# Kernel tuning notes

Measured on AMD Instinct MI355X. Metric: run time of the kernel, lower is better.

## Reference

```python
import jax, jax.numpy as jnp
import numpy as np

NUM_HEAD = 2
KR = 3          # kernel_range = [3, 3]
SHIFT = 1
N_P = KR * KR   # 9 taps
PAD = (KR // 2) * SHIFT  # 1
OFFSETS = [(i, j) for i in (-(KR // 2), 0, KR // 2) if True for j in ()]  # placeholder, real list below
OFFSETS = [(i, j) for i in range(-(KR // 2), KR // 2 + 1) for j in range(-(KR // 2), KR // 2 + 1)]


def _conv3x3(x, w, b):
    # x: [B,H,W,Cin], w: [3,3,Cin,Cout] -> SAME conv + bias
    y = jax.lax.conv_general_dilated(
        x, w, window_strides=(1, 1), padding='SAME',
        dimension_numbers=('NHWC', 'HWIO', 'NHWC'))
    return y + b


def setup_inputs() -> dict:
    key = jax.random.key(0)
    B, H, W, D = 4, 128, 128, 64
    ks = jax.random.split(key, 10)
    sc = 0.05  # small init like glorot
    return {
        'x': jax.random.normal(ks[0], (B, H, W, D), jnp.float32),
        # 1x1 conv kernels stored as matrices (equiv. to (1,1,Cin,Cout))
        'K_P': jax.random.normal(ks[1], (D, D * N_P), jnp.float32) * sc,
        'V_P': jax.random.normal(ks[2], (D, D * N_P), jnp.float32) * sc,
        'Q_P': jax.random.normal(ks[3], (D, D), jnp.float32) * sc,
        'ff1_kernel': jax.random.normal(ks[4], (D, D), jnp.float32) * sc,
        'ff1_bias': jax.random.normal(ks[5], (D,), jnp.float32) * sc,
        'ff2_kernel': jax.random.normal(ks[6], (3, 3, D, 2 * D), jnp.float32) * sc,
        'ff2_bias': jax.random.normal(ks[7], (2 * D,), jnp.float32) * sc,
        'ff3_kernel': jax.random.normal(ks[8], (3, 3, 2 * D, D), jnp.float32) * sc,
        'ff3_bias': jax.random.normal(ks[9], (D,), jnp.float32) * sc,
    }


def reference(x, K_P, V_P, Q_P, ff1_kernel, ff1_bias, ff2_kernel, ff2_bias,
              ff3_kernel, ff3_bias):
    B, H, W, D = x.shape
    hd = D // NUM_HEAD

    # 1x1 projections; K/V produce N_P channel chunks, one per tap
    x_k = jnp.einsum('bhwd,de->bhwe', x, K_P).reshape(B, H, W, N_P, D)
    x_v = jnp.einsum('bhwd,de->bhwe', x, V_P).reshape(B, H, W, N_P, D)
    x_q = jnp.einsum('bhwd,de->bhwe', x, Q_P)

    pad5 = ((0, 0), (PAD, PAD), (PAD, PAD), (0, 0), (0, 0))
    k_pad = jnp.pad(x_k, pad5)
    v_pad = jnp.pad(x_v, pad5)

    # tap t uses channel chunk t at spatial offset OFFSETS[t]*SHIFT
    def taps(padded):
        return jnp.stack(
            [padded[:, PAD + i * SHIFT:PAD + i * SHIFT + H,
                    PAD + j * SHIFT:PAD + j * SHIFT + W, t, :]
             for t, (i, j) in enumerate(OFFSETS)], axis=3)  # [B,H,W,N_P,D]

    k_taps = taps(k_pad)
    v_taps = taps(v_pad)

    # validity mask (padded taps get score 0 before softmax, as in original)
    m_pad = jnp.pad(jnp.ones((B, H, W), x.dtype), ((0, 0), (PAD, PAD), (PAD, PAD)))
    mask = jnp.stack(
        [m_pad[:, PAD + i * SHIFT:PAD + i * SHIFT + H,
               PAD + j * SHIFT:PAD + j * SHIFT + W]
         for (i, j) in OFFSETS], axis=3)  # [B,H,W,N_P]

    kh = k_taps.reshape(B, H, W, N_P, NUM_HEAD, hd)
    vh = v_taps.reshape(B, H, W, N_P, NUM_HEAD, hd)
    qh = x_q.reshape(B, H, W, NUM_HEAD, hd)

    # scores per head over taps; masked-multiply then /3, as in original
    scores = jnp.einsum('bhwtnc,bhwnc->bhwnt', kh, qh)
    scores = scores * mask[:, :, :, None, :] / 3.0
    alpha = jax.nn.softmax(scores, axis=-1)  # over taps
    attn = jnp.einsum('bhwnt,bhwtnc->bhwnc', alpha, vh).reshape(B, H, W, D)

    # FFN: 1x1 conv -> relu -> 3x3 conv -> relu -> 3x3 conv -> relu
    t = jax.nn.relu(jnp.einsum('bhwd,de->bhwe', attn, ff1_kernel) + ff1_bias)
    t = jax.nn.relu(_conv3x3(t, ff2_kernel, ff2_bias))
    t = jax.nn.relu(_conv3x3(t, ff3_kernel, ff3_bias))
    return t
```

## Files before the change

kernel.cpp:

```cpp
#include <hip/hip_runtime.h>


typedef _Float16 half8 __attribute__((ext_vector_type(8)));
typedef _Float16 half4v __attribute__((ext_vector_type(4)));
typedef float f32x4 __attribute__((ext_vector_type(4)));

__device__ __forceinline__ f32x4 mfma16(half8 a, half8 b, f32x4 c) {
  return __builtin_amdgcn_mfma_f32_16x16x32_f16(a, b, c, 0, 0, 0);
}
__device__ __forceinline__ half8 ldfrag(const _Float16* p) { return *(const half8*)p; }
__device__ __forceinline__ half8 zfrag() { half8 z = {}; return z; }

__device__ __forceinline__ void gload_lds16(const _Float16* g, _Float16* l) {
  __builtin_amdgcn_global_load_lds(
      (const __attribute__((address_space(1))) void*)g,
      (__attribute__((address_space(3))) void*)l, 16, 0, 0);
}

__global__ __launch_bounds__(256) void prep(
    const float* __restrict__ x, const float* __restrict__ Kp,
    const float* __restrict__ Vp, const float* __restrict__ Qp,
    const float* __restrict__ W1, const float* __restrict__ F2,
    const float* __restrict__ F3, _Float16* __restrict__ xh,
    _Float16* __restrict__ out) {
  if (blockIdx.x < 4096) {
    int i = blockIdx.x * 256 + threadIdx.x;
    float4 v = ((const float4*)x)[i];
    half4v h = { (_Float16)v.x, (_Float16)v.y, (_Float16)v.z, (_Float16)v.w };
    *(half4v*)(xh + i * 4) = h;
    return;
  }
  int e = (blockIdx.x - 4096) * 256 + threadIdx.x;
  int j = e & 7, l = (e >> 3) & 63, f = e >> 9;
  int l15 = l & 15, q8 = (l >> 4) * 8;
  float v;
  if (f < 8)        { int mb = f >> 1, kb = f & 1;
                      v = Qp[(kb*32 + q8 + j) * 64 + mb*16 + l15]; }
  else if (f < 80)  { int g = f - 8, t = g >> 3, mb = (g >> 1) & 3, kb = g & 1;
                      v = Kp[(kb*32 + q8 + j) * 576 + t*64 + mb*16 + l15]; }
  else if (f < 152) { int g = f - 80, t = g >> 3, kb = (g >> 2) & 1, nb = g & 3;
                      v = Vp[(kb*32 + q8 + j) * 576 + t*64 + nb*16 + l15]; }
  else if (f < 160) { int g = f - 152, kb = g >> 2, nb = g & 3;
                      v = W1[(kb*32 + q8 + j) * 64 + nb*16 + l15]; }
  else if (f < 304) { int g = f - 160, t = g >> 4, kb = (g >> 3) & 1, nb = g & 7;
                      v = F2[(t*64 + kb*32 + q8 + j) * 128 + nb*16 + l15]; }
  else              { int g = f - 304, t = g >> 4, kb = (g >> 2) & 3, nb = g & 3;
                      v = F3[(t*128 + kb*32 + q8 + j) * 64 + nb*16 + l15]; }
  out[e] = (_Float16)v;
}

__global__ __launch_bounds__(512) void attn_ff1(
    const _Float16* __restrict__ xh, const _Float16* __restrict__ wf,
    const float* __restrict__ f1b, _Float16* __restrict__ t1g) {
  extern __shared__ _Float16 smem[];
  const int lane = threadIdx.x & 63, wid = threadIdx.x >> 6;
  const int l15 = lane & 15, q8 = (lane >> 4) * 8;
  const int row = blockIdx.x * 2 + (wid >> 2);
  const int rw = wid & 3;
  const int p0 = row * 128 + rw * 32;
  const int h = row & 127;
  const int w0 = rw * 32;
  float* dent = (float*)(smem + 77824) + wid * 64;

  {
    const _Float16* gw = wf + 4096 + (size_t)(wid * 19) * 512;
    _Float16* lw = smem + wid * 19 * 512;
    for (int i = 0; i < 19; ++i)
      gload_lds16(gw + i * 512 + lane * 8, lw + i * 512);
  }

  half8 ax0[2], ax1[2];
#pragma unroll
  for (int m = 0; m < 2; ++m) {
    const _Float16* xp = xh + (size_t)(p0 + m * 16 + l15) * 64 + q8;
    ax0[m] = ldfrag(xp); ax1[m] = ldfrag(xp + 32);
  }
  f32x4 qT[2][4];
#pragma unroll
  for (int cb = 0; cb < 4; ++cb) {
    half8 aq0 = ldfrag(wf + (cb * 2 + 0) * 512 + lane * 8);
    half8 aq1 = ldfrag(wf + (cb * 2 + 1) * 512 + lane * 8);
#pragma unroll
    for (int m = 0; m < 2; ++m) {
      f32x4 c = {};
      c = mfma16(aq0, ax0[m], c);
      c = mfma16(aq1, ax1[m], c);
      qT[m][cb] = c;
    }
  }

  auto load_tap = [&](int t, half8 (&x0)[2], half8 (&x1)[2]) {
    const int dh = t / 3 - 1, dw = t % 3 - 1;
    const bool rk = (unsigned)(h + dh) < 128u;
#pragma unroll
    for (int m = 0; m < 2; ++m) {
      const bool cv = rk && ((unsigned)(w0 + m * 16 + l15 + dw) < 128u);
      const _Float16* sp = xh + (size_t)(p0 + m * 16 + l15 + dh * 128 + dw) * 64 + q8;
      x0[m] = cv ? ldfrag(sp) : zfrag();
      x1[m] = cv ? ldfrag(sp + 32) : zfrag();
    }
  };

  float den0[2] = {0.f, 0.f}, den1[2] = {0.f, 0.f};
  auto score_tap = [&](int t, half8 (&x0)[2], half8 (&x1)[2],
                       float (&e0)[2], float (&e1)[2]) {
    const int dh = t / 3 - 1;
    const bool rowok = (unsigned)(h + dh) < 128u;
#pragma unroll
    for (int m = 0; m < 2; ++m) {
      float pa = 0.f, pb = 0.f;
      if (rowok) {
#pragma unroll
        for (int cb = 0; cb < 4; ++cb) {
          f32x4 c = {};
          c = mfma16(ldfrag(smem + (t * 8 + cb * 2 + 0) * 512 + lane * 8), x0[m], c);
          c = mfma16(ldfrag(smem + (t * 8 + cb * 2 + 1) * 512 + lane * 8), x1[m], c);
          float d = qT[m][cb].x * c.x + qT[m][cb].y * c.y
                  + qT[m][cb].z * c.z + qT[m][cb].w * c.w;
          if (cb < 2) pa += d; else pb += d;
        }
        pa += __shfl_xor(pa, 16, 64); pa += __shfl_xor(pa, 32, 64);
        pb += __shfl_xor(pb, 16, 64); pb += __shfl_xor(pb, 32, 64);
      }
      e0[m] = __expf(pa * (1.f / 3.f));
      e1[m] = __expf(pb * (1.f / 3.f));
      den0[m] += e0[m]; den1[m] += e1[m];
    }
  };

  half8 sx0[2], sx1[2];
  load_tap(0, sx0, sx1);

  __syncthreads();

  float e0c[2], e1c[2];
  score_tap(0, sx0, sx1, e0c, e1c);

  const _Float16* BVl = smem + 36864;
  f32x4 at[2][4];
#pragma unroll
  for (int m = 0; m < 2; ++m)
#pragma unroll
    for (int nb = 0; nb < 4; ++nb) at[m][nb] = f32x4{};

#pragma unroll
  for (int t = 0; t < 9; ++t) {
    const bool rowok = (unsigned)(h + (t / 3 - 1)) < 128u;
    half8 nx0[2], nx1[2];
    if (t < 8) load_tap(t + 1, nx0, nx1);
    if (rowok) {
      half8 vf[8];
#pragma unroll
      for (int f = 0; f < 8; ++f) vf[f] = ldfrag(BVl + (t * 8 + f) * 512 + lane * 8);
#pragma unroll
      for (int m = 0; m < 2; ++m) {
        _Float16 h0 = (_Float16)e0c[m], h1 = (_Float16)e1c[m];
        half8 b0 = {h0, h0, h0, h0, h0, h0, h0, h0};
        half8 b1 = {h1, h1, h1, h1, h1, h1, h1, h1};
        half8 s00 = sx0[m] * b0, s01 = sx1[m] * b0;
        half8 s10 = sx0[m] * b1, s11 = sx1[m] * b1;
#pragma unroll
        for (int nb = 0; nb < 2; ++nb) {
          at[m][nb]     = mfma16(s00, vf[0 * 4 + nb],     at[m][nb]);
          at[m][nb]     = mfma16(s01, vf[1 * 4 + nb],     at[m][nb]);
          at[m][nb + 2] = mfma16(s10, vf[0 * 4 + nb + 2], at[m][nb + 2]);
          at[m][nb + 2] = mfma16(s11, vf[1 * 4 + nb + 2], at[m][nb + 2]);
        }
      }
    }
    if (t < 8) {
      float e0n[2], e1n[2];
      score_tap(t + 1, nx0, nx1, e0n, e1n);
#pragma unroll
      for (int m = 0; m < 2; ++m) {
        sx0[m] = nx0[m]; sx1[m] = nx1[m];
        e0c[m] = e0n[m]; e1c[m] = e1n[m];
      }
    }
  }

#pragma unroll
  for (int m = 0; m < 2; ++m) {
    dent[(m * 2 + 0) * 16 + l15] = den0[m];
    dent[(m * 2 + 1) * 16 + l15] = den1[m];
  }
  f32x4 iv[2][2];
#pragma unroll
  for (int m = 0; m < 2; ++m)
#pragma unroll
    for (int hd = 0; hd < 2; ++hd) {
      f32x4 dv = *(const f32x4*)(dent + (m * 2 + hd) * 16 + (lane >> 4) * 4);
      iv[m][hd] = f32x4{1.f / dv.x, 1.f / dv.y, 1.f / dv.z, 1.f / dv.w};
    }

  __syncthreads();
  _Float16* myt = smem + wid * 2304;
#pragma unroll
  for (int m = 0; m < 2; ++m)
#pragma unroll
    for (int nb = 0; nb < 4; ++nb) {
      const int hd = nb >> 1;
#pragma unroll
      for (int r = 0; r < 4; ++r)
        myt[m * 1152 + ((lane >> 4) * 4 + r) * 72 + nb * 16 + l15] =
            (_Float16)(at[m][nb][r] * iv[m][hd][r]);
    }
  const _Float16* B1l = smem + 73728;
#pragma unroll
  for (int m = 0; m < 2; ++m) {
    half8 aa0 = ldfrag(myt + m * 1152 + l15 * 72 + q8);
    half8 aa1 = ldfrag(myt + m * 1152 + l15 * 72 + 32 + q8);
#pragma unroll
    for (int nb = 0; nb < 4; ++nb) {
      f32x4 c = {};
      c = mfma16(aa0, ldfrag(B1l + (0 * 4 + nb) * 512 + lane * 8), c);
      c = mfma16(aa1, ldfrag(B1l + (1 * 4 + nb) * 512 + lane * 8), c);
      float bv = f1b[nb * 16 + l15];
#pragma unroll
      for (int r = 0; r < 4; ++r) {
        float v = fmaxf(c[r] + bv, 0.f);
        t1g[(size_t)(p0 + m * 16 + (lane >> 4) * 4 + r) * 64 + nb * 16 + l15] = (_Float16)v;
      }
    }
  }
}

template <int KB, int NBL, int COUT>
__global__ __launch_bounds__(512, 2) void conv3x3(
    const _Float16* __restrict__ in, const _Float16* __restrict__ wfrag,
    const float* __restrict__ bias, void* __restrict__ outp, int out_fp32) {
  extern __shared__ _Float16 smem[];
  const int lane = threadIdx.x & 63, wid = threadIdx.x >> 6;
  const int l15 = lane & 15, q8 = (lane >> 4) * 8;
  const int nh = blockIdx.x & 1;
  const int pairIdx = blockIdx.x >> 1;
  const int row = pairIdx * 2 + (wid >> 2);
  const int rw = wid & 3;
  const int p0 = row * 128 + rw * 32;
  const int h = row & 127;
  const int w0 = rw * 32;
  const int CIN = KB * 32;
  const int NBF = COUT / 16;

  {
    for (int s = 0; s < 9; ++s) {
      int f = wid * 9 + s;
      int t = f >> 3, r = f & 7, kb = r / NBL, i = r % NBL;
      const _Float16* g = wfrag + (size_t)((t * KB + kb) * NBF + nh * NBL + i) * 512;
      gload_lds16(g + lane * 8, smem + f * 512);
    }
  }

  f32x4 acc[2][NBL];
#pragma unroll
  for (int m = 0; m < 2; ++m)
#pragma unroll
    for (int nb = 0; nb < NBL; ++nb) acc[m][nb] = f32x4{};

  half8 a[2][KB];
  {
    const bool rk = (unsigned)(h - 1) < 128u;
#pragma unroll
    for (int m = 0; m < 2; ++m) {
      const bool cv = rk && ((unsigned)(w0 + m * 16 + l15 - 1) < 128u);
      const _Float16* sp = in + (size_t)(p0 + m * 16 + l15 - 129) * CIN + q8;
#pragma unroll
      for (int kb = 0; kb < KB; ++kb) a[m][kb] = cv ? ldfrag(sp + kb * 32) : zfrag();
    }
  }

  __syncthreads();

#pragma unroll
  for (int t = 0; t < 9; ++t) {
    const int dh = t / 3 - 1;
    const bool rowok = (unsigned)(h + dh) < 128u;
    half8 an[2][KB];
    if (t < 8) {
      const int dh2 = (t + 1) / 3 - 1, dw2 = (t + 1) % 3 - 1;
      const bool rk2 = (unsigned)(h + dh2) < 128u;
#pragma unroll
      for (int m = 0; m < 2; ++m) {
        const bool cv = rk2 && ((unsigned)(w0 + m * 16 + l15 + dw2) < 128u);
        const _Float16* sp = in + (size_t)(p0 + m * 16 + l15 + dh2 * 128 + dw2) * CIN + q8;
#pragma unroll
        for (int kb = 0; kb < KB; ++kb) an[m][kb] = cv ? ldfrag(sp + kb * 32) : zfrag();
      }
    }
    if (rowok) {
#pragma unroll
      for (int nb = 0; nb < NBL; ++nb) {
#pragma unroll
        for (int kb = 0; kb < KB; ++kb) {
          half8 b = ldfrag(smem + (size_t)((t * KB + kb) * NBL + nb) * 512 + lane * 8);
          acc[0][nb] = mfma16(a[0][kb], b, acc[0][nb]);
          acc[1][nb] = mfma16(a[1][kb], b, acc[1][nb]);
        }
      }
    }
    if (t < 8) {
#pragma unroll
      for (int m = 0; m < 2; ++m)
#pragma unroll
        for (int kb = 0; kb < KB; ++kb) a[m][kb] = an[m][kb];
    }
  }

#pragma unroll
  for (int m = 0; m < 2; ++m)
#pragma unroll
    for (int nb = 0; nb < NBL; ++nb) {
      float bv = bias[nh * NBL * 16 + nb * 16 + l15];
#pragma unroll
      for (int r = 0; r < 4; ++r) {
        float v = fmaxf(acc[m][nb][r] + bv, 0.f);
        size_t idx = (size_t)(p0 + m * 16 + (lane >> 4) * 4 + r) * COUT
                   + nh * NBL * 16 + nb * 16 + l15;
        if (out_fp32) ((float*)outp)[idx] = v;
        else          ((_Float16*)outp)[idx] = (_Float16)v;
      }
    }
}

extern "C" void kernel_launch(void* const* d_in, const int* in_sizes, int n_in,
                              void* d_out, int out_size, void* d_ws, size_t ws_size,
                              hipStream_t stream) {
  (void)in_sizes; (void)n_in; (void)out_size; (void)ws_size;
  const float* x   = (const float*)d_in[0];
  const float* Kp  = (const float*)d_in[1];
  const float* Vp  = (const float*)d_in[2];
  const float* Qp  = (const float*)d_in[3];
  const float* f1w = (const float*)d_in[4];
  const float* f1b = (const float*)d_in[5];
  const float* f2w = (const float*)d_in[6];
  const float* f2b = (const float*)d_in[7];
  const float* f3w = (const float*)d_in[8];
  const float* f3b = (const float*)d_in[9];

  _Float16* xh  = (_Float16*)d_ws;
  _Float16* wf  = xh + 4194304;
  _Float16* t2g = wf + 229376;
  _Float16* t1g = (_Float16*)d_out;

  (void)hipFuncSetAttribute((const void*)attn_ff1,
      hipFuncAttributeMaxDynamicSharedMemorySize, 157696);
  (void)hipFuncSetAttribute((const void*)conv3x3<2, 4, 128>,
      hipFuncAttributeMaxDynamicSharedMemorySize, 73728);
  (void)hipFuncSetAttribute((const void*)conv3x3<4, 2, 64>,
      hipFuncAttributeMaxDynamicSharedMemorySize, 73728);

  prep<<<4992, 256, 0, stream>>>(x, Kp, Vp, Qp, f1w, f2w, f3w, xh, wf);
  attn_ff1<<<256, 512, 157696, stream>>>(xh, wf, f1b, t1g);
  conv3x3<2, 4, 128><<<512, 512, 73728, stream>>>(t1g, wf + 81920, f2b, t2g, 0);
  conv3x3<4, 2, 64><<<512, 512, 73728, stream>>>(t2g, wf + 155648, f3b, d_out, 1);
}
```

Measured before the change: 166.0 us.

## Fuse all four stages into one cooperative persistent kernel with grid syncs

Replaces the four separate launches (prep, attention+ff1, two 3x3 convs) with one cooperative kernel of 256 blocks that runs each stage in turn, separated by grid-wide syncs. This removes launch gaps and inter-kernel drain. Each conv stage now has one block compute all output channels for two rows, where before two blocks split the channels, which halves parallelism in the conv stages. With 157KB of LDS per block the grid runs at one block per CU, so occupancy drops and the grid syncs add their own overhead.

Result: slower. 255.6 us (+53.9%).

```diff
diff --git a/kernel.cpp b/kernel.cpp
--- a/kernel.cpp
+++ b/kernel.cpp
@@ -1,4 +1,6 @@
 #include <hip/hip_runtime.h>
+#include <hip/hip_cooperative_groups.h>
+namespace cg = cooperative_groups;
 
 
 typedef _Float16 half8 __attribute__((ext_vector_type(8)));
@@ -17,41 +19,102 @@
       (__attribute__((address_space(3))) void*)l, 16, 0, 0);
 }
 
-__global__ __launch_bounds__(256) void prep(
+template <int KB, int NB, bool OUT_FP32>
+__device__ __forceinline__ void conv_stage(
+    _Float16* smem, const _Float16* __restrict__ in,
+    const _Float16* __restrict__ wfrag, const float* __restrict__ bias,
+    void* __restrict__ outp, int lane, int wid, int row, int rw) {
+  const int l15 = lane & 15, q8 = (lane >> 4) * 8;
+  const int p0 = row * 128 + rw * 32;
+  const int h = row & 127;
+  const int w0 = rw * 32;
+  const int CIN = KB * 32, COUT = NB * 16;
+
+#pragma unroll
+  for (int i = 0; i < 18; ++i) {
+    int f = wid * 18 + i;
+    gload_lds16(wfrag + (size_t)f * 512 + lane * 8, smem + f * 512);
+  }
+
+  f32x4 acc[2][NB];
+#pragma unroll
+  for (int m = 0; m < 2; ++m)
+#pragma unroll
+    for (int nb = 0; nb < NB; ++nb) acc[m][nb] = f32x4{};
+
+  half8 a[2][KB];
+  {
+    const bool rk = (unsigned)(h - 1) < 128u;
+#pragma unroll
+    for (int m = 0; m < 2; ++m) {
+      const bool cv = rk && ((unsigned)(w0 + m * 16 + l15 - 1) < 128u);
+      const _Float16* sp = in + (size_t)(p0 + m * 16 + l15 - 129) * CIN + q8;
+#pragma unroll
+      for (int kb = 0; kb < KB; ++kb) a[m][kb] = cv ? ldfrag(sp + kb * 32) : zfrag();
+    }
+  }
+
+  __syncthreads();
+
+#pragma unroll
+  for (int t = 0; t < 9; ++t) {
+    const int dh = t / 3 - 1;
+    const bool rowok = (unsigned)(h + dh) < 128u;
+    half8 an[2][KB];
+    if (t < 8) {
+      const int dh2 = (t + 1) / 3 - 1, dw2 = (t + 1) % 3 - 1;
+      const bool rk2 = (unsigned)(h + dh2) < 128u;
+#pragma unroll
+      for (int m = 0; m < 2; ++m) {
+        const bool cv = rk2 && ((unsigned)(w0 + m * 16 + l15 + dw2) < 128u);
+        const _Float16* sp = in + (size_t)(p0 + m * 16 + l15 + dh2 * 128 + dw2) * CIN + q8;
+#pragma unroll
+        for (int kb = 0; kb < KB; ++kb) an[m][kb] = cv ? ldfrag(sp + kb * 32) : zfrag();
+      }
+    }
+    if (rowok) {
+#pragma unroll
+      for (int nb = 0; nb < NB; ++nb) {
+#pragma unroll
+        for (int kb = 0; kb < KB; ++kb) {
+          half8 b = ldfrag(smem + (size_t)((t * KB + kb) * NB + nb) * 512 + lane * 8);
+          acc[0][nb] = mfma16(a[0][kb], b, acc[0][nb]);
+          acc[1][nb] = mfma16(a[1][kb], b, acc[1][nb]);
+        }
+      }
+    }
+    if (t < 8) {
+#pragma unroll
+      for (int m = 0; m < 2; ++m)
+#pragma unroll
+        for (int kb = 0; kb < KB; ++kb) a[m][kb] = an[m][kb];
+    }
+  }
+
+#pragma unroll
+  for (int m = 0; m < 2; ++m)
+#pragma unroll
+    for (int nb = 0; nb < NB; ++nb) {
+      float bv = bias[nb * 16 + l15];
+#pragma unroll
+      for (int r = 0; r < 4; ++r) {
+        float v = fmaxf(acc[m][nb][r] + bv, 0.f);
+        size_t idx = (size_t)(p0 + m * 16 + (lane >> 4) * 4 + r) * COUT + nb * 16 + l15;
+        if (OUT_FP32) ((float*)outp)[idx] = v;
+        else          ((_Float16*)outp)[idx] = (_Float16)v;
+      }
+    }
+}
+
+__global__ __launch_bounds__(512) void fused(
     const float* __restrict__ x, const float* __restrict__ Kp,
     const float* __restrict__ Vp, const float* __restrict__ Qp,
-    const float* __restrict__ W1, const float* __restrict__ F2,
-    const float* __restrict__ F3, _Float16* __restrict__ xh,
-    _Float16* __restrict__ out) {
-  if (blockIdx.x < 4096) {
-    int i = blockIdx.x * 256 + threadIdx.x;
-    float4 v = ((const float4*)x)[i];
-    half4v h = { (_Float16)v.x, (_Float16)v.y, (_Float16)v.z, (_Float16)v.w };
-    *(half4v*)(xh + i * 4) = h;
-    return;
-  }
-  int e = (blockIdx.x - 4096) * 256 + threadIdx.x;
-  int j = e & 7, l = (e >> 3) & 63, f = e >> 9;
-  int l15 = l & 15, q8 = (l >> 4) * 8;
-  float v;
-  if (f < 8)        { int mb = f >> 1, kb = f & 1;
-                      v = Qp[(kb*32 + q8 + j) * 64 + mb*16 + l15]; }
-  else if (f < 80)  { int g = f - 8, t = g >> 3, mb = (g >> 1) & 3, kb = g & 1;
-                      v = Kp[(kb*32 + q8 + j) * 576 + t*64 + mb*16 + l15]; }
-  else if (f < 152) { int g = f - 80, t = g >> 3, kb = (g >> 2) & 1, nb = g & 3;
-                      v = Vp[(kb*32 + q8 + j) * 576 + t*64 + nb*16 + l15]; }
-  else if (f < 160) { int g = f - 152, kb = g >> 2, nb = g & 3;
-                      v = W1[(kb*32 + q8 + j) * 64 + nb*16 + l15]; }
-  else if (f < 304) { int g = f - 160, t = g >> 4, kb = (g >> 3) & 1, nb = g & 7;
-                      v = F2[(t*64 + kb*32 + q8 + j) * 128 + nb*16 + l15]; }
-  else              { int g = f - 304, t = g >> 4, kb = (g >> 2) & 3, nb = g & 3;
-                      v = F3[(t*128 + kb*32 + q8 + j) * 64 + nb*16 + l15]; }
-  out[e] = (_Float16)v;
-}
-
-__global__ __launch_bounds__(512) void attn_ff1(
-    const _Float16* __restrict__ xh, const _Float16* __restrict__ wf,
-    const float* __restrict__ f1b, _Float16* __restrict__ t1g) {
+    const float* __restrict__ W1, const float* __restrict__ f1b,
+    const float* __restrict__ F2, const float* __restrict__ f2b,
+    const float* __restrict__ F3, const float* __restrict__ f3b,
+    _Float16* __restrict__ xh, _Float16* __restrict__ wf,
+    _Float16* __restrict__ t1g, _Float16* __restrict__ t2g,
+    float* __restrict__ outp) {
   extern __shared__ _Float16 smem[];
   const int lane = threadIdx.x & 63, wid = threadIdx.x >> 6;
   const int l15 = lane & 15, q8 = (lane >> 4) * 8;
@@ -60,266 +123,213 @@
   const int p0 = row * 128 + rw * 32;
   const int h = row & 127;
   const int w0 = rw * 32;
-  float* dent = (float*)(smem + 77824) + wid * 64;
+  const int gtid = blockIdx.x * 512 + threadIdx.x;
 
   {
-    const _Float16* gw = wf + 4096 + (size_t)(wid * 19) * 512;
-    _Float16* lw = smem + wid * 19 * 512;
-    for (int i = 0; i < 19; ++i)
-      gload_lds16(gw + i * 512 + lane * 8, lw + i * 512);
-  }
-
-  half8 ax0[2], ax1[2];
-#pragma unroll
-  for (int m = 0; m < 2; ++m) {
-    const _Float16* xp = xh + (size_t)(p0 + m * 16 + l15) * 64 + q8;
-    ax0[m] = ldfrag(xp); ax1[m] = ldfrag(xp + 32);
-  }
-  f32x4 qT[2][4];
-#pragma unroll
-  for (int cb = 0; cb < 4; ++cb) {
-    half8 aq0 = ldfrag(wf + (cb * 2 + 0) * 512 + lane * 8);
-    half8 aq1 = ldfrag(wf + (cb * 2 + 1) * 512 + lane * 8);
+    const float4* x4 = (const float4*)x;
+#pragma unroll
+    for (int k = 0; k < 8; ++k) {
+      int i = gtid + k * 131072;
+      float4 v = x4[i];
+      half4v hv = { (_Float16)v.x, (_Float16)v.y, (_Float16)v.z, (_Float16)v.w };
+      *(half4v*)(xh + (size_t)i * 4) = hv;
+    }
+#pragma unroll
+    for (int k = 0; k < 2; ++k) {
+      int e = gtid + k * 131072;
+      if (e < 229376) {
+        int j = e & 7, l = (e >> 3) & 63, f = e >> 9;
+        int ll = l & 15, qq = (l >> 4) * 8;
+        float v;
+        if (f < 8)        { int mb = f >> 1, kb = f & 1;
+                            v = Qp[(kb*32 + qq + j) * 64 + mb*16 + ll]; }
+        else if (f < 80)  { int g = f - 8, t = g >> 3, mb = (g >> 1) & 3, kb = g & 1;
+                            v = Kp[(kb*32 + qq + j) * 576 + t*64 + mb*16 + ll]; }
+        else if (f < 152) { int g = f - 80, t = g >> 3, kb = (g >> 2) & 1, nb = g & 3;
+                            v = Vp[(kb*32 + qq + j) * 576 + t*64 + nb*16 + ll]; }
+        else if (f < 160) { int g = f - 152, kb = g >> 2, nb = g & 3;
+                            v = W1[(kb*32 + qq + j) * 64 + nb*16 + ll]; }
+        else if (f < 304) { int g = f - 160, t = g >> 4, kb = (g >> 3) & 1, nb = g & 7;
+                            v = F2[(t*64 + kb*32 + qq + j) * 128 + nb*16 + ll]; }
+        else              { int g = f - 304, t = g >> 4, kb = (g >> 2) & 3, nb = g & 3;
+                            v = F3[(t*128 + kb*32 + qq + j) * 64 + nb*16 + ll]; }
+        wf[e] = (_Float16)v;
+      }
+    }
+  }
+  cg::this_grid().sync();
+
+  {
+    float* dent = (float*)(smem + 77824) + wid * 64;
+
+    {
+      const _Float16* gw = wf + 4096 + (size_t)(wid * 19) * 512;
+      _Float16* lw = smem + wid * 19 * 512;
+      for (int i = 0; i < 19; ++i)
+        gload_lds16(gw + i * 512 + lane * 8, lw + i * 512);
+    }
+
+    half8 ax0[2], ax1[2];
 #pragma unroll
     for (int m = 0; m < 2; ++m) {
-      f32x4 c = {};
-      c = mfma16(aq0, ax0[m], c);
-      c = mfma16(aq1, ax1[m], c);
-      qT[m][cb] = c;
-    }
-  }
-
-  auto load_tap = [&](int t, half8 (&x0)[2], half8 (&x1)[2]) {
-    const int dh = t / 3 - 1, dw = t % 3 - 1;
-    const bool rk = (unsigned)(h + dh) < 128u;
+      const _Float16* xp = xh + (size_t)(p0 + m * 16 + l15) * 64 + q8;
+      ax0[m] = ldfrag(xp); ax1[m] = ldfrag(xp + 32);
+    }
+    f32x4 qT[2][4];
+#pragma unroll
+    for (int cb = 0; cb < 4; ++cb) {
+      half8 aq0 = ldfrag(wf + (cb * 2 + 0) * 512 + lane * 8);
+      half8 aq1 = ldfrag(wf + (cb * 2 + 1) * 512 + lane * 8);
+#pragma unroll
+      for (int m = 0; m < 2; ++m) {
+        f32x4 c = {};
+        c = mfma16(aq0, ax0[m], c);
+        c = mfma16(aq1, ax1[m], c);
+        qT[m][cb] = c;
+      }
+    }
+
+    auto load_tap = [&](int t, half8 (&x0)[2], half8 (&x1)[2]) {
+      const int dh = t / 3 - 1, dw = t % 3 - 1;
+      const bool rk = (unsigned)(h + dh) < 128u;
+#pragma unroll
+      for (int m = 0; m < 2; ++m) {
+        const bool cv = rk && ((unsigned)(w0 + m * 16 + l15 + dw) < 128u);
+        const _Float16* sp = xh + (size_t)(p0 + m * 16 + l15 + dh * 128 + dw) * 64 + q8;
+        x0[m] = cv ? ldfrag(sp) : zfrag();
+        x1[m] = cv ? ldfrag(sp + 32) : zfrag();
+      }
+    };
+
+    float den0[2] = {0.f, 0.f}, den1[2] = {0.f, 0.f};
+    auto score_tap = [&](int t, half8 (&x0)[2], half8 (&x1)[2],
+                         float (&e0)[2], float (&e1)[2]) {
+      const int dh = t / 3 - 1;
+      const bool rowok = (unsigned)(h + dh) < 128u;
+#pragma unroll
+      for (int m = 0; m < 2; ++m) {
+        float pa = 0.f, pb = 0.f;
+        if (rowok) {
+#pragma unroll
+          for (int cb = 0; cb < 4; ++cb) {
+            f32x4 c = {};
+            c = mfma16(ldfrag(smem + (t * 8 + cb * 2 + 0) * 512 + lane * 8), x0[m], c);
+            c = mfma16(ldfrag(smem + (t * 8 + cb * 2 + 1) * 512 + lane * 8), x1[m], c);
+            float d = qT[m][cb].x * c.x + qT[m][cb].y * c.y
+                    + qT[m][cb].z * c.z + qT[m][cb].w * c.w;
+            if (cb < 2) pa += d; else pb += d;
+          }
+          pa += __shfl_xor(pa, 16, 64); pa += __shfl_xor(pa, 32, 64);
+          pb += __shfl_xor(pb, 16, 64); pb += __shfl_xor(pb, 32, 64);
+        }
+        e0[m] = __expf(pa * (1.f / 3.f));
+        e1[m] = __expf(pb * (1.f / 3.f));
+        den0[m] += e0[m]; den1[m] += e1[m];
+      }
+    };
+
+    half8 sx0[2], sx1[2];
+    load_tap(0, sx0, sx1);
+
+    __syncthreads();
+
+    float e0c[2], e1c[2];
+    score_tap(0, sx0, sx1, e0c, e1c);
+
+    const _Float16* BVl = smem + 36864;
+    f32x4 at[2][4];
+#pragma unroll
+    for (int m = 0; m < 2; ++m)
+#pragma unroll
+      for (int nb = 0; nb < 4; ++nb) at[m][nb] = f32x4{};
+
+#pragma unroll
+    for (int t = 0; t < 9; ++t) {
+      const bool rowok = (unsigned)(h + (t / 3 - 1)) < 128u;
+      half8 nx0[2], nx1[2];
+      if (t < 8) load_tap(t + 1, nx0, nx1);
+      if (rowok) {
+        half8 vf[8];
+#pragma unroll
+        for (int f = 0; f < 8; ++f) vf[f] = ldfrag(BVl + (t * 8 + f) * 512 + lane * 8);
+#pragma unroll
+        for (int m = 0; m < 2; ++m) {
+          _Float16 h0 = (_Float16)e0c[m], h1 = (_Float16)e1c[m];
+          half8 b0 = {h0, h0, h0, h0, h0, h0, h0, h0};
+          half8 b1 = {h1, h1, h1, h1, h1, h1, h1, h1};
+          half8 s00 = sx0[m] * b0, s01 = sx1[m] * b0;
+          half8 s10 = sx0[m] * b1, s11 = sx1[m] * b1;
+#pragma unroll
+          for (int nb = 0; nb < 2; ++nb) {
+            at[m][nb]     = mfma16(s00, vf[0 * 4 + nb],     at[m][nb]);
+            at[m][nb]     = mfma16(s01, vf[1 * 4 + nb],     at[m][nb]);
+            at[m][nb + 2] = mfma16(s10, vf[0 * 4 + nb + 2], at[m][nb + 2]);
+            at[m][nb + 2] = mfma16(s11, vf[1 * 4 + nb + 2], at[m][nb + 2]);
+          }
+        }
+      }
+      if (t < 8) {
+        float e0n[2], e1n[2];
+        score_tap(t + 1, nx0, nx1, e0n, e1n);
+#pragma unroll
+        for (int m = 0; m < 2; ++m) {
+          sx0[m] = nx0[m]; sx1[m] = nx1[m];
+          e0c[m] = e0n[m]; e1c[m] = e1n[m];
+        }
+      }
+    }
+
 #pragma unroll
     for (int m = 0; m < 2; ++m) {
-      const bool cv = rk && ((unsigned)(w0 + m * 16 + l15 + dw) < 128u);
-      const _Float16* sp = xh + (size_t)(p0 + m * 16 + l15 + dh * 128 + dw) * 64 + q8;
-      x0[m] = cv ? ldfrag(sp) : zfrag();
-      x1[m] = cv ? ldfrag(sp + 32) : zfrag();
-    }
-  };
-
-  float den0[2] = {0.f, 0.f}, den1[2] = {0.f, 0.f};
-  auto score_tap = [&](int t, half8 (&x0)[2], half8 (&x1)[2],
-                       float (&e0)[2], float (&e1)[2]) {
-    const int dh = t / 3 - 1;
-    const bool rowok = (unsigned)(h + dh) < 128u;
+      dent[(m * 2 + 0) * 16 + l15] = den0[m];
+      dent[(m * 2 + 1) * 16 + l15] = den1[m];
+    }
+    f32x4 iv[2][2];
+#pragma unroll
+    for (int m = 0; m < 2; ++m)
+#pragma unroll
+      for (int hd = 0; hd < 2; ++hd) {
+        f32x4 dv = *(const f32x4*)(dent + (m * 2 + hd) * 16 + (lane >> 4) * 4);
+        iv[m][hd] = f32x4{1.f / dv.x, 1.f / dv.y, 1.f / dv.z, 1.f / dv.w};
+      }
+
+    __syncthreads();
+    _Float16* myt = smem + wid * 2304;
+#pragma unroll
+    for (int m = 0; m < 2; ++m)
+#pragma unroll
+      for (int nb = 0; nb < 4; ++nb) {
+        const int hd = nb >> 1;
+#pragma unroll
+        for (int r = 0; r < 4; ++r)
+          myt[m * 1152 + ((lane >> 4) * 4 + r) * 72 + nb * 16 + l15] =
+              (_Float16)(at[m][nb][r] * iv[m][hd][r]);
+      }
+    const _Float16* B1l = smem + 73728;
 #pragma unroll
     for (int m = 0; m < 2; ++m) {
-      float pa = 0.f, pb = 0.f;
-      if (rowok) {
-#pragma unroll
-        for (int cb = 0; cb < 4; ++cb) {
-          f32x4 c = {};
-          c = mfma16(ldfrag(smem + (t * 8 + cb * 2 + 0) * 512 + lane * 8), x0[m], c);
-          c = mfma16(ldfrag(smem + (t * 8 + cb * 2 + 1) * 512 + lane * 8), x1[m], c);
-          float d = qT[m][cb].x * c.x + qT[m][cb].y * c.y
-                  + qT[m][cb].z * c.z + qT[m][cb].w * c.w;
-          if (cb < 2) pa += d; else pb += d;
-        }
-        pa += __shfl_xor(pa, 16, 64); pa += __shfl_xor(pa, 32, 64);
-        pb += __shfl_xor(pb, 16, 64); pb += __shfl_xor(pb, 32, 64);
-      }
-      e0[m] = __expf(pa * (1.f / 3.f));
-      e1[m] = __expf(pb * (1.f / 3.f));
-      den0[m] += e0[m]; den1[m] += e1[m];
-    }
-  };
-
-  half8 sx0[2], sx1[2];
-  load_tap(0, sx0, sx1);
-
-  __syncthreads();
-
-  float e0c[2], e1c[2];
-  score_tap(0, sx0, sx1, e0c, e1c);
-
-  const _Float16* BVl = smem + 36864;
-  f32x4 at[2][4];
-#pragma unroll
-  for (int m = 0; m < 2; ++m)
-#pragma unroll
-    for (int nb = 0; nb < 4; ++nb) at[m][nb] = f32x4{};
-
-#pragma unroll
-  for (int t = 0; t < 9; ++t) {
-    const bool rowok = (unsigned)(h + (t / 3 - 1)) < 128u;
-    half8 nx0[2], nx1[2];
-    if (t < 8) load_tap(t + 1, nx0, nx1);
-    if (rowok) {
-      half8 vf[8];
-#pragma unroll
-      for (int f = 0; f < 8; ++f) vf[f] = ldfrag(BVl + (t * 8 + f) * 512 + lane * 8);
-#pragma unroll
-      for (int m = 0; m < 2; ++m) {
-        _Float16 h0 = (_Float16)e0c[m], h1 = (_Float16)e1c[m];
-        half8 b0 = {h0, h0, h0, h0, h0, h0, h0, h0};
-        half8 b1 = {h1, h1, h1, h1, h1, h1, h1, h1};
-        half8 s00 = sx0[m] * b0, s01 = sx1[m] * b0;
-        half8 s10 = sx0[m] * b1, s11 = sx1[m] * b1;
-#pragma unroll
-        for (int nb = 0; nb < 2; ++nb) {
-          at[m][nb]     = mfma16(s00, vf[0 * 4 + nb],     at[m][nb]);
-          at[m][nb]     = mfma16(s01, vf[1 * 4 + nb],     at[m][nb]);
-          at[m][nb + 2] = mfma16(s10, vf[0 * 4 + nb + 2], at[m][nb + 2]);
-          at[m][nb + 2] = mfma16(s11, vf[1 * 4 + nb + 2], at[m][nb + 2]);
-        }
-      }
-    }
-    if (t < 8) {
-      float e0n[2], e1n[2];
-      score_tap(t + 1, nx0, nx1, e0n, e1n);
-#pragma unroll
-      for (int m = 0; m < 2; ++m) {
-        sx0[m] = nx0[m]; sx1[m] = nx1[m];
-        e0c[m] = e0n[m]; e1c[m] = e1n[m];
-      }
-    }
-  }
-
-#pragma unroll
-  for (int m = 0; m < 2; ++m) {
-    dent[(m * 2 + 0) * 16 + l15] = den0[m];
-    dent[(m * 2 + 1) * 16 + l15] = den1[m];
-  }
-  f32x4 iv[2][2];
-#pragma unroll
-  for (int m = 0; m < 2; ++m)
-#pragma unroll
-    for (int hd = 0; hd < 2; ++hd) {
-      f32x4 dv = *(const f32x4*)(dent + (m * 2 + hd) * 16 + (lane >> 4) * 4);
-      iv[m][hd] = f32x4{1.f / dv.x, 1.f / dv.y, 1.f / dv.z, 1.f / dv.w};
-    }
-
-  __syncthreads();
-  _Float16* myt = smem + wid * 2304;
-#pragma unroll
-  for (int m = 0; m < 2; ++m)
-#pragma unroll
-    for (int nb = 0; nb < 4; ++nb) {
-      const int hd = nb >> 1;
-#pragma unroll
-      for (int r = 0; r < 4; ++r)
-        myt[m * 1152 + ((lane >> 4) * 4 + r) * 72 + nb * 16 + l15] =
-            (_Float16)(at[m][nb][r] * iv[m][hd][r]);
-    }
-  const _Float16* B1l = smem + 73728;
-#pragma unroll
-  for (int m = 0; m < 2; ++m) {
-    half8 aa0 = ldfrag(myt + m * 1152 + l15 * 72 + q8);
-    half8 aa1 = ldfrag(myt + m * 1152 + l15 * 72 + 32 + q8);
-#pragma unroll
-    for (int nb = 0; nb < 4; ++nb) {
-      f32x4 c = {};
-      c = mfma16(aa0, ldfrag(B1l + (0 * 4 + nb) * 512 + lane * 8), c);
-      c = mfma16(aa1, ldfrag(B1l + (1 * 4 + nb) * 512 + lane * 8), c);
-      float bv = f1b[nb * 16 + l15];
-#pragma unroll
-      for (int r = 0; r < 4; ++r) {
-        float v = fmaxf(c[r] + bv, 0.f);
-        t1g[(size_t)(p0 + m * 16 + (lane >> 4) * 4 + r) * 64 + nb * 16 + l15] = (_Float16)v;
-      }
-    }
-  }
-}
-
-template <int KB, int NBL, int COUT>
-__global__ __launch_bounds__(512, 2) void conv3x3(
-    const _Float16* __restrict__ in, const _Float16* __restrict__ wfrag,
-    const float* __restrict__ bias, void* __restrict__ outp, int out_fp32) {
-  extern __shared__ _Float16 smem[];
-  const int lane = threadIdx.x & 63, wid = threadIdx.x >> 6;
-  const int l15 = lane & 15, q8 = (lane >> 4) * 8;
-  const int nh = blockIdx.x & 1;
-  const int pairIdx = blockIdx.x >> 1;
-  const int row = pairIdx * 2 + (wid >> 2);
-  const int rw = wid & 3;
-  const int p0 = row * 128 + rw * 32;
-  const int h = row & 127;
-  const int w0 = rw * 32;
-  const int CIN = KB * 32;
-  const int NBF = COUT / 16;
-
-  {
-    for (int s = 0; s < 9; ++s) {
-      int f = wid * 9 + s;
-      int t = f >> 3, r = f & 7, kb = r / NBL, i = r % NBL;
-      const _Float16* g = wfrag + (size_t)((t * KB + kb) * NBF + nh * NBL + i) * 512;
-      gload_lds16(g + lane * 8, smem + f * 512);
-    }
-  }
-
-  f32x4 acc[2][NBL];
-#pragma unroll
-  for (int m = 0; m < 2; ++m)
-#pragma unroll
-    for (int nb = 0; nb < NBL; ++nb) acc[m][nb] = f32x4{};
-
-  half8 a[2][KB];
-  {
-    const bool rk = (unsigned)(h - 1) < 128u;
-#pragma unroll
-    for (int m = 0; m < 2; ++m) {
-      const bool cv = rk && ((unsigned)(w0 + m * 16 + l15 - 1) < 128u);
-      const _Float16* sp = in + (size_t)(p0 + m * 16 + l15 - 129) * CIN + q8;
-#pragma unroll
-      for (int kb = 0; kb < KB; ++kb) a[m][kb] = cv ? ldfrag(sp + kb * 32) : zfrag();
-    }
-  }
-
-  __syncthreads();
-
-#pragma unroll
-  for (int t = 0; t < 9; ++t) {
-    const int dh = t / 3 - 1;
-    const bool rowok = (unsigned)(h + dh) < 128u;
-    half8 an[2][KB];
-    if (t < 8) {
-      const int dh2 = (t + 1) / 3 - 1, dw2 = (t + 1) % 3 - 1;
-      const bool rk2 = (unsigned)(h + dh2) < 128u;
-#pragma unroll
-      for (int m = 0; m < 2; ++m) {
-        const bool cv = rk2 && ((unsigned)(w0 + m * 16 + l15 + dw2) < 128u);
-        const _Float16* sp = in + (size_t)(p0 + m * 16 + l15 + dh2 * 128 + dw2) * CIN + q8;
-#pragma unroll
-        for (int kb = 0; kb < KB; ++kb) an[m][kb] = cv ? ldfrag(sp + kb * 32) : zfrag();
-      }
-    }
-    if (rowok) {
-#pragma unroll
-      for (int nb = 0; nb < NBL; ++nb) {
-#pragma unroll
-        for (int kb = 0; kb < KB; ++kb) {
-          half8 b = ldfrag(smem + (size_t)((t * KB + kb) * NBL + nb) * 512 + lane * 8);
-          acc[0][nb] = mfma16(a[0][kb], b, acc[0][nb]);
-          acc[1][nb] = mfma16(a[1][kb], b, acc[1][nb]);
-        }
-      }
-    }
-    if (t < 8) {
-#pragma unroll
-      for (int m = 0; m < 2; ++m)
-#pragma unroll
-        for (int kb = 0; kb < KB; ++kb) a[m][kb] = an[m][kb];
-    }
-  }
-
-#pragma unroll
-  for (int m = 0; m < 2; ++m)
-#pragma unroll
-    for (int nb = 0; nb < NBL; ++nb) {
-      float bv = bias[nh * NBL * 16 + nb * 16 + l15];
-#pragma unroll
-      for (int r = 0; r < 4; ++r) {
-        float v = fmaxf(acc[m][nb][r] + bv, 0.f);
-        size_t idx = (size_t)(p0 + m * 16 + (lane >> 4) * 4 + r) * COUT
-                   + nh * NBL * 16 + nb * 16 + l15;
-        if (out_fp32) ((float*)outp)[idx] = v;
-        else          ((_Float16*)outp)[idx] = (_Float16)v;
-      }
-    }
+      half8 aa0 = ldfrag(myt + m * 1152 + l15 * 72 + q8);
+      half8 aa1 = ldfrag(myt + m * 1152 + l15 * 72 + 32 + q8);
+#pragma unroll
+      for (int nb = 0; nb < 4; ++nb) {
+        f32x4 c = {};
+        c = mfma16(aa0, ldfrag(B1l + (0 * 4 + nb) * 512 + lane * 8), c);
+        c = mfma16(aa1, ldfrag(B1l + (1 * 4 + nb) * 512 + lane * 8), c);
+        float bv = f1b[nb * 16 + l15];
+#pragma unroll
+        for (int r = 0; r < 4; ++r) {
+          float v = fmaxf(c[r] + bv, 0.f);
+          t1g[(size_t)(p0 + m * 16 + (lane >> 4) * 4 + r) * 64 + nb * 16 + l15] = (_Float16)v;
+        }
+      }
+    }
+  }
+  cg::this_grid().sync();
+
+  conv_stage<2, 8, false>(smem, t1g, wf + 81920, f2b, t2g, lane, wid, row, rw);
+  cg::this_grid().sync();
+
+  conv_stage<4, 4, true>(smem, t2g, wf + 155648, f3b, outp, lane, wid, row, rw);
 }
 
 extern "C" void kernel_launch(void* const* d_in, const int* in_sizes, int n_in,
@@ -340,17 +350,16 @@
   _Float16* xh  = (_Float16*)d_ws;
   _Float16* wf  = xh + 4194304;
   _Float16* t2g = wf + 229376;
-  _Float16* t1g = (_Float16*)d_out;
-
-  (void)hipFuncSetAttribute((const void*)attn_ff1,
+  _Float16* t1g = t2g + 8388608;
+  float* outp = (float*)d_out;
+
+  (void)hipFuncSetAttribute((const void*)fused,
       hipFuncAttributeMaxDynamicSharedMemorySize, 157696);
-  (void)hipFuncSetAttribute((const void*)conv3x3<2, 4, 128>,
-      hipFuncAttributeMaxDynamicSharedMemorySize, 73728);
-  (void)hipFuncSetAttribute((const void*)conv3x3<4, 2, 64>,
-      hipFuncAttributeMaxDynamicSharedMemorySize, 73728);
-
-  prep<<<4992, 256, 0, stream>>>(x, Kp, Vp, Qp, f1w, f2w, f3w, xh, wf);
-  attn_ff1<<<256, 512, 157696, stream>>>(xh, wf, f1b, t1g);
-  conv3x3<2, 4, 128><<<512, 512, 73728, stream>>>(t1g, wf + 81920, f2b, t2g, 0);
-  conv3x3<4, 2, 64><<<512, 512, 73728, stream>>>(t2g, wf + 155648, f3b, d_out, 1);
-}
+
+  void* args[] = { (void*)&x, (void*)&Kp, (void*)&Vp, (void*)&Qp, (void*)&f1w,
+                   (void*)&f1b, (void*)&f2w, (void*)&f2b, (void*)&f3w,
+                   (void*)&f3b, (void*)&xh, (void*)&wf, (void*)&t1g,
+                   (void*)&t2g, (void*)&outp };
+  (void)hipLaunchCooperativeKernel((const void*)fused, dim3(256), dim3(512),
+                                   args, 157696, stream);
+}
```

## Store fp16 activations in channel-octet planar layout for coalesced fragment loads

Applied to the files above, without the earlier changes.

Fp16 activation buffers (x, t1, t2) move from NHWC to a layout of 8-channel planes, so each MFMA fragment load of 8 channels reads consecutive 16-byte chunks across neighbouring pixels. The prep conversion, the attention kernel's loads and stores, and both conv kernels' input loads and fp16 output stores are rewritten for this layout. t1 now lives in workspace instead of the output buffer. The epilogue stores become 2-byte scattered writes with stride 8 halves, which may hurt store efficiency.

Measured after the change: 147.2 us. -11.3%, faster.

```diff
diff --git a/kernel.cpp b/kernel.cpp
--- a/kernel.cpp
+++ b/kernel.cpp
@@ -2,8 +2,9 @@
 
 
 typedef _Float16 half8 __attribute__((ext_vector_type(8)));
-typedef _Float16 half4v __attribute__((ext_vector_type(4)));
 typedef float f32x4 __attribute__((ext_vector_type(4)));
+
+#define PLANE 524288
 
 __device__ __forceinline__ f32x4 mfma16(half8 a, half8 b, f32x4 c) {
   return __builtin_amdgcn_mfma_f32_16x16x32_f16(a, b, c, 0, 0, 0);
@@ -23,14 +24,17 @@
     const float* __restrict__ W1, const float* __restrict__ F2,
     const float* __restrict__ F3, _Float16* __restrict__ xh,
     _Float16* __restrict__ out) {
-  if (blockIdx.x < 4096) {
+  if (blockIdx.x < 2048) {
     int i = blockIdx.x * 256 + threadIdx.x;
-    float4 v = ((const float4*)x)[i];
-    half4v h = { (_Float16)v.x, (_Float16)v.y, (_Float16)v.z, (_Float16)v.w };
-    *(half4v*)(xh + i * 4) = h;
+    int oct = i >> 16, px = i & 65535;
+    const float4* s = (const float4*)(x + (size_t)px * 64 + oct * 8);
+    float4 a = s[0], b = s[1];
+    half8 h = { (_Float16)a.x, (_Float16)a.y, (_Float16)a.z, (_Float16)a.w,
+                (_Float16)b.x, (_Float16)b.y, (_Float16)b.z, (_Float16)b.w };
+    *(half8*)(xh + (size_t)oct * PLANE + (size_t)px * 8) = h;
     return;
   }
-  int e = (blockIdx.x - 4096) * 256 + threadIdx.x;
+  int e = (blockIdx.x - 2048) * 256 + threadIdx.x;
   int j = e & 7, l = (e >> 3) & 63, f = e >> 9;
   int l15 = l & 15, q8 = (l >> 4) * 8;
   float v;
@@ -60,6 +64,7 @@
   const int p0 = row * 128 + rw * 32;
   const int h = row & 127;
   const int w0 = rw * 32;
+  const int oct0 = lane >> 4;
   float* dent = (float*)(smem + 77824) + wid * 64;
 
   {
@@ -72,8 +77,9 @@
   half8 ax0[2], ax1[2];
 #pragma unroll
   for (int m = 0; m < 2; ++m) {
-    const _Float16* xp = xh + (size_t)(p0 + m * 16 + l15) * 64 + q8;
-    ax0[m] = ldfrag(xp); ax1[m] = ldfrag(xp + 32);
+    const size_t px = (size_t)(p0 + m * 16 + l15);
+    ax0[m] = ldfrag(xh + (size_t)oct0 * PLANE + px * 8);
+    ax1[m] = ldfrag(xh + (size_t)(oct0 + 4) * PLANE + px * 8);
   }
   f32x4 qT[2][4];
 #pragma unroll
@@ -95,9 +101,9 @@
 #pragma unroll
     for (int m = 0; m < 2; ++m) {
       const bool cv = rk && ((unsigned)(w0 + m * 16 + l15 + dw) < 128u);
-      const _Float16* sp = xh + (size_t)(p0 + m * 16 + l15 + dh * 128 + dw) * 64 + q8;
-      x0[m] = cv ? ldfrag(sp) : zfrag();
-      x1[m] = cv ? ldfrag(sp + 32) : zfrag();
+      const size_t px = (size_t)(p0 + m * 16 + l15 + dh * 128 + dw);
+      x0[m] = cv ? ldfrag(xh + (size_t)oct0 * PLANE + px * 8) : zfrag();
+      x1[m] = cv ? ldfrag(xh + (size_t)(oct0 + 4) * PLANE + px * 8) : zfrag();
     }
   };
 
@@ -216,10 +222,13 @@
       c = mfma16(aa0, ldfrag(B1l + (0 * 4 + nb) * 512 + lane * 8), c);
       c = mfma16(aa1, ldfrag(B1l + (1 * 4 + nb) * 512 + lane * 8), c);
       float bv = f1b[nb * 16 + l15];
+      const int ch = nb * 16 + l15;
+      const size_t pbase = (size_t)(ch >> 3) * PLANE + (ch & 7);
 #pragma unroll
       for (int r = 0; r < 4; ++r) {
         float v = fmaxf(c[r] + bv, 0.f);
-        t1g[(size_t)(p0 + m * 16 + (lane >> 4) * 4 + r) * 64 + nb * 16 + l15] = (_Float16)v;
+        size_t px = (size_t)(p0 + m * 16 + (lane >> 4) * 4 + r);
+        t1g[pbase + px * 8] = (_Float16)v;
       }
     }
   }
@@ -239,8 +248,8 @@
   const int p0 = row * 128 + rw * 32;
   const int h = row & 127;
   const int w0 = rw * 32;
-  const int CIN = KB * 32;
   const int NBF = COUT / 16;
+  const int oct0 = lane >> 4;
 
   {
     for (int s = 0; s < 9; ++s) {
@@ -263,9 +272,10 @@
 #pragma unroll
     for (int m = 0; m < 2; ++m) {
       const bool cv = rk && ((unsigned)(w0 + m * 16 + l15 - 1) < 128u);
-      const _Float16* sp = in + (size_t)(p0 + m * 16 + l15 - 129) * CIN + q8;
-#pragma unroll
-      for (int kb = 0; kb < KB; ++kb) a[m][kb] = cv ? ldfrag(sp + kb * 32) : zfrag();
+      const size_t px = (size_t)(p0 + m * 16 + l15 - 129);
+#pragma unroll
+      for (int kb = 0; kb < KB; ++kb)
+        a[m][kb] = cv ? ldfrag(in + (size_t)(kb * 4 + oct0) * PLANE + px * 8) : zfrag();
     }
   }
 
@@ -282,9 +292,10 @@
 #pragma unroll
       for (int m = 0; m < 2; ++m) {
         const bool cv = rk2 && ((unsigned)(w0 + m * 16 + l15 + dw2) < 128u);
-        const _Float16* sp = in + (size_t)(p0 + m * 16 + l15 + dh2 * 128 + dw2) * CIN + q8;
-#pragma unroll
-        for (int kb = 0; kb < KB; ++kb) an[m][kb] = cv ? ldfrag(sp + kb * 32) : zfrag();
+        const size_t px = (size_t)(p0 + m * 16 + l15 + dh2 * 128 + dw2);
+#pragma unroll
+        for (int kb = 0; kb < KB; ++kb)
+          an[m][kb] = cv ? ldfrag(in + (size_t)(kb * 4 + oct0) * PLANE + px * 8) : zfrag();
       }
     }
     if (rowok) {
@@ -310,14 +321,17 @@
   for (int m = 0; m < 2; ++m)
 #pragma unroll
     for (int nb = 0; nb < NBL; ++nb) {
-      float bv = bias[nh * NBL * 16 + nb * 16 + l15];
+      const int ch = nh * NBL * 16 + nb * 16 + l15;
+      float bv = bias[ch];
 #pragma unroll
       for (int r = 0; r < 4; ++r) {
         float v = fmaxf(acc[m][nb][r] + bv, 0.f);
-        size_t idx = (size_t)(p0 + m * 16 + (lane >> 4) * 4 + r) * COUT
-                   + nh * NBL * 16 + nb * 16 + l15;
-        if (out_fp32) ((float*)outp)[idx] = v;
-        else          ((_Float16*)outp)[idx] = (_Float16)v;
+        size_t px = (size_t)(p0 + m * 16 + (lane >> 4) * 4 + r);
+        if (out_fp32) {
+          ((float*)outp)[px * COUT + ch] = v;
+        } else {
+          ((_Float16*)outp)[(size_t)(ch >> 3) * PLANE + px * 8 + (ch & 7)] = (_Float16)v;
+        }
       }
     }
 }
@@ -339,8 +353,9 @@
 
   _Float16* xh  = (_Float16*)d_ws;
   _Float16* wf  = xh + 4194304;
-  _Float16* t2g = wf + 229376;
-  _Float16* t1g = (_Float16*)d_out;
+  _Float16* t1g = wf + 229376;
+  _Float16* t2g = t1g + 4194304;
+  float* outp = (float*)d_out;
 
   (void)hipFuncSetAttribute((const void*)attn_ff1,
       hipFuncAttributeMaxDynamicSharedMemorySize, 157696);
@@ -349,8 +364,8 @@
   (void)hipFuncSetAttribute((const void*)conv3x3<4, 2, 64>,
       hipFuncAttributeMaxDynamicSharedMemorySize, 73728);
 
-  prep<<<4992, 256, 0, stream>>>(x, Kp, Vp, Qp, f1w, f2w, f3w, xh, wf);
+  prep<<<2944, 256, 0, stream>>>(x, Kp, Vp, Qp, f1w, f2w, f3w, xh, wf);
   attn_ff1<<<256, 512, 157696, stream>>>(xh, wf, f1b, t1g);
   conv3x3<2, 4, 128><<<512, 512, 73728, stream>>>(t1g, wf + 81920, f2b, t2g, 0);
-  conv3x3<4, 2, 64><<<512, 512, 73728, stream>>>(t2g, wf + 155648, f3b, d_out, 1);
-}
+  conv3x3<4, 2, 64><<<512, 512, 73728, stream>>>(t2g, wf + 155648, f3b, outp, 1);
+}
```
